# Optimization experiments

Measured on AMD Instinct MI355X. Metric: run time of the kernel, lower is better.

Reference implementation:

```python
import jax, jax.numpy as jnp
import numpy as np

N, H, G, D, FF, R = 16384, 32, 8, 128, 2, 4
GROUPS = H // G            # n_head = heads per kv group
NBAND = D // (2 * FF)      # 32


def _fold_k(t):
    # t: [N, G, D] -> (real, imag) each [N, NBAND, G*FF]; mirrors torch transpose/reshape order
    Df = D // 2
    t = jnp.swapaxes(t, -1, -2)  # [N, D, G]
    def fold(x):  # x: [N, Df, G]
        x = x.reshape(-1, NBAND, FF, G)
        x = jnp.swapaxes(x, 1, 2)          # [N, FF, NBAND, G]
        return x.reshape(-1, NBAND, G * FF)
    return fold(t[:, :Df, :]), fold(t[:, Df:, :])


def _fold_q(t):
    # t: [N, H, D] -> (real, imag) each [N, GROUPS, NBAND, G*FF]
    Df = D // 2
    t = t.reshape(-1, G, GROUPS, D).transpose(0, 2, 1, 3)  # [N, GROUPS, G, D]
    t = jnp.swapaxes(t, -1, -2)                            # [N, GROUPS, D, G]
    def fold(x):  # x: [N, GROUPS, Df, G]
        x = x.reshape(-1, GROUPS, NBAND, FF, G)
        x = jnp.swapaxes(x, 2, 3)                          # [N, GROUPS, FF, NBAND, G]
        return x.reshape(-1, GROUPS, NBAND, G * FF)
    return fold(t[:, :, :Df, :]), fold(t[:, :, Df:, :])


def setup_inputs() -> dict:
    key = jax.random.key(0)
    ks = jax.random.split(key, 5)
    return {
        "q": jax.random.normal(ks[0], (N, H, D), jnp.float32),
        "k": jax.random.normal(ks[1], (N, G, D), jnp.float32),
        "v": jax.random.normal(ks[2], (N, G, D), jnp.float32),
        "qk_index_proj": 0.02 * jax.random.normal(ks[3], (NBAND, G * FF, FF), jnp.float32),
        "v_transform": 0.02 * jax.random.normal(ks[4], (H, D, R), jnp.float32),
    }


def reference(q, k, v, qk_index_proj, v_transform):
    # index_k: fold K, project per-band, concat real/imag -> [N, D]
    kr_re, kr_im = _fold_k(k)
    kr_re_p = jnp.einsum('bnf,nfr->bnr', kr_re, qk_index_proj)
    kr_im_p = jnp.einsum('bnf,nfr->bnr', kr_im, qk_index_proj)
    index_k = jnp.concatenate(
        [kr_re_p.reshape(-1, NBAND * FF), kr_im_p.reshape(-1, NBAND * FF)], axis=-1)

    # index_q: fold Q, project per-band, concat real/imag -> [N, GROUPS, D]
    qr_re, qr_im = _fold_q(q)
    qr_re_p = jnp.einsum('tgnf,nfr->tgnr', qr_re, qk_index_proj)
    qr_im_p = jnp.einsum('tgnf,nfr->tgnr', qr_im, qk_index_proj)
    index_q = jnp.concatenate(
        [qr_re_p.reshape(-1, GROUPS, NBAND * FF), qr_im_p.reshape(-1, GROUPS, NBAND * FF)], axis=-1)

    # weights: low-rank V transform + L2 norm -> [N, GROUPS]
    v_h = jnp.repeat(v, GROUPS, axis=1)                     # [N, H, D]
    w = jnp.einsum('nhd,hdr->nhr', v_h, v_transform)        # [N, H, R]
    w = w.reshape(-1, G, GROUPS, R).transpose(0, 2, 1, 3).reshape(-1, GROUPS, G * R)
    weights = jnp.linalg.norm(w.astype(jnp.float32), axis=-1)
    return index_q, index_k, weights
```

## Files before the change

kernel.cpp:

```cpp
#include <hip/hip_runtime.h>

#define NN 16384
#define HH 32
#define GG 8
#define DD 128
#define RR 4
#define NGROUPS 4
#define NBAND 32


__global__ __launch_bounds__(256) void idxer_kernel(
    const float* __restrict__ q, const float* __restrict__ k,
    const float* __restrict__ v, const float* __restrict__ proj,
    const float* __restrict__ vt, float* __restrict__ out)
{
    const int b = blockIdx.x;
    const int tid = threadIdx.x;

    __shared__ float sq[HH * DD];
    __shared__ float sk[GG * DD];
    __shared__ float sv[GG * DD];
    __shared__ float sproj[NBAND * 33];
    __shared__ float sw[HH];

    {
        const float4* q4 = (const float4*)(q + (size_t)b * (HH * DD));
        float4* s4 = (float4*)sq;
        #pragma unroll
        for (int i = 0; i < 4; ++i) s4[tid + 256 * i] = q4[tid + 256 * i];
        const float4* k4 = (const float4*)(k + (size_t)b * (GG * DD));
        ((float4*)sk)[tid] = k4[tid];
        const float4* v4 = (const float4*)(v + (size_t)b * (GG * DD));
        ((float4*)sv)[tid] = v4[tid];
        #pragma unroll
        for (int i = 0; i < 4; ++i) {
            int p = tid + 256 * i;
            sproj[(p >> 5) * 33 + (p & 31)] = proj[p];
        }
    }
    __syncthreads();

    {
        const int group = tid >> 6;
        const int im = (tid >> 5) & 1;
        const int n = tid & 31;
        const int dbase = (n & 15) * 4 + (n >> 4) + im * 64;
        float acc0 = 0.f, acc1 = 0.f;
        #pragma unroll
        for (int j = 0; j < 16; ++j) {
            const int d = dbase + (j >> 3) * 2;
            const int head = (j & 7) * 4 + group;
            const float qv = sq[head * DD + d];
            acc0 += qv * sproj[n * 33 + j * 2];
            acc1 += qv * sproj[n * 33 + j * 2 + 1];
        }
        float2* o2 = (float2*)out;
        o2[(size_t)b * 256 + group * 64 + im * 32 + n] = make_float2(acc0, acc1);
    }

    if (tid < 64) {
        const int im = tid >> 5;
        const int n = tid & 31;
        const int dbase = (n & 15) * 4 + (n >> 4) + im * 64;
        float acc0 = 0.f, acc1 = 0.f;
        #pragma unroll
        for (int j = 0; j < 16; ++j) {
            const int d = dbase + (j >> 3) * 2;
            const int g = j & 7;
            const float kv = sk[g * DD + d];
            acc0 += kv * sproj[n * 33 + j * 2];
            acc1 += kv * sproj[n * 33 + j * 2 + 1];
        }
        float2* o2 = (float2*)(out + (size_t)NN * 512);
        o2[(size_t)b * 64 + im * 32 + n] = make_float2(acc0, acc1);
    }

    {
        const int h = tid >> 3;
        const int s = tid & 7;
        const int g = h >> 2;
        const float4* vt4 = (const float4*)vt;
        float a0 = 0.f, a1 = 0.f, a2 = 0.f, a3 = 0.f;
        #pragma unroll
        for (int i = 0; i < 16; ++i) {
            const int d = i * 8 + s;
            const float4 w4 = vt4[h * DD + d];
            const float vv = sv[g * DD + d];
            a0 += vv * w4.x; a1 += vv * w4.y; a2 += vv * w4.z; a3 += vv * w4.w;
        }
        #pragma unroll
        for (int off = 4; off >= 1; off >>= 1) {
            a0 += __shfl_down(a0, off, 8);
            a1 += __shfl_down(a1, off, 8);
            a2 += __shfl_down(a2, off, 8);
            a3 += __shfl_down(a3, off, 8);
        }
        if (s == 0) sw[h] = a0 * a0 + a1 * a1 + a2 * a2 + a3 * a3;
    }
    __syncthreads();

    if (tid < NGROUPS) {
        float acc = 0.f;
        #pragma unroll
        for (int g = 0; g < 8; ++g) acc += sw[g * 4 + tid];
        out[(size_t)NN * 512 + (size_t)NN * 128 + (size_t)b * 4 + tid] = sqrtf(acc);
    }
}

extern "C" void kernel_launch(void* const* d_in, const int* in_sizes, int n_in,
                              void* d_out, int out_size, void* d_ws, size_t ws_size,
                              hipStream_t stream) {
    const float* q    = (const float*)d_in[0];
    const float* k    = (const float*)d_in[1];
    const float* v    = (const float*)d_in[2];
    const float* proj = (const float*)d_in[3];
    const float* vt   = (const float*)d_in[4];
    float* out = (float*)d_out;
    idxer_kernel<<<NN, 256, 0, stream>>>(q, k, v, proj, vt, out);
}
```

Before: 447.1 us.

## Process eight tokens per block, stream q/k from global, reuse proj and v_transform

Each block now handles eight tokens instead of one. The per-token setup cost (loading the proj table and the v_transform slice held in registers) is paid once per block rather than once per token. Q and K are read directly from global memory as float4 into registers instead of being staged through shared memory, and only V is staged. The final cross-head reduction for the weights uses wave shuffles instead of a second barrier and shared-memory pass. In exchange, each thread does more serial work, the grid has fewer blocks, and register pressure rises from holding 16 float4 values.

```diff
diff --git a/kernel.cpp b/kernel.cpp
--- a/kernel.cpp
+++ b/kernel.cpp
@@ -1,12 +1,8 @@
 #include <hip/hip_runtime.h>
 
 #define NN 16384
-#define HH 32
-#define GG 8
-#define DD 128
-#define RR 4
-#define NGROUPS 4
-#define NBAND 32
+#define TT 8
+#define NBLK (NN / TT)
 
 
 __global__ __launch_bounds__(256) void idxer_kernel(
@@ -14,96 +10,118 @@
     const float* __restrict__ v, const float* __restrict__ proj,
     const float* __restrict__ vt, float* __restrict__ out)
 {
-    const int b = blockIdx.x;
     const int tid = threadIdx.x;
+    const int t0 = blockIdx.x * TT;
 
-    __shared__ float sq[HH * DD];
-    __shared__ float sk[GG * DD];
-    __shared__ float sv[GG * DD];
-    __shared__ float sproj[NBAND * 33];
-    __shared__ float sw[HH];
+    __shared__ __align__(16) float sproj[32 * 34];
+    __shared__ __align__(16) float sv[TT][8 * 132];
 
     {
-        const float4* q4 = (const float4*)(q + (size_t)b * (HH * DD));
-        float4* s4 = (float4*)sq;
+        const float4* pv4 = (const float4*)v;
+        float4 vbuf[TT];
         #pragma unroll
-        for (int i = 0; i < 4; ++i) s4[tid + 256 * i] = q4[tid + 256 * i];
-        const float4* k4 = (const float4*)(k + (size_t)b * (GG * DD));
-        ((float4*)sk)[tid] = k4[tid];
-        const float4* v4 = (const float4*)(v + (size_t)b * (GG * DD));
-        ((float4*)sv)[tid] = v4[tid];
+        for (int t = 0; t < TT; ++t)
+            vbuf[t] = pv4[(size_t)(t0 + t) * 256 + tid];
+        float pbuf[4];
+        #pragma unroll
+        for (int i = 0; i < 4; ++i) pbuf[i] = proj[tid + 256 * i];
         #pragma unroll
         for (int i = 0; i < 4; ++i) {
-            int p = tid + 256 * i;
-            sproj[(p >> 5) * 33 + (p & 31)] = proj[p];
+            const int p = tid + 256 * i;
+            sproj[(p >> 5) * 34 + (p & 31)] = pbuf[i];
         }
+        const int g = tid >> 5;
+        const int rem = (tid & 31) * 4;
+        #pragma unroll
+        for (int t = 0; t < TT; ++t)
+            *(float4*)&sv[t][g * 132 + rem] = vbuf[t];
     }
     __syncthreads();
 
     {
-        const int group = tid >> 6;
-        const int im = (tid >> 5) & 1;
-        const int n = tid & 31;
-        const int dbase = (n & 15) * 4 + (n >> 4) + im * 64;
-        float acc0 = 0.f, acc1 = 0.f;
-        #pragma unroll
-        for (int j = 0; j < 16; ++j) {
-            const int d = dbase + (j >> 3) * 2;
-            const int head = (j & 7) * 4 + group;
-            const float qv = sq[head * DD + d];
-            acc0 += qv * sproj[n * 33 + j * 2];
-            acc1 += qv * sproj[n * 33 + j * 2 + 1];
+        const int half = tid >> 7;
+        const int lt = tid & 127;
+        const int group = lt >> 5;
+        const int im = (lt >> 4) & 1;
+        const int a = lt & 15;
+        float2* o2 = (float2*)out;
+        #pragma unroll 2
+        for (int tq = 0; tq < TT / 2; ++tq) {
+            const int b = t0 + tq * 2 + half;
+            const float4* q4 = (const float4*)(q + (size_t)b * 4096);
+            float a0 = 0.f, a1 = 0.f, c0 = 0.f, c1 = 0.f;
+            #pragma unroll
+            for (int g8 = 0; g8 < 8; ++g8) {
+                const float4 qv = q4[(g8 * 4 + group) * 32 + im * 16 + a];
+                const float2 pa  = *(const float2*)&sproj[a * 34 + g8 * 2];
+                const float2 pa2 = *(const float2*)&sproj[a * 34 + 16 + g8 * 2];
+                const float2 pb  = *(const float2*)&sproj[(a + 16) * 34 + g8 * 2];
+                const float2 pb2 = *(const float2*)&sproj[(a + 16) * 34 + 16 + g8 * 2];
+                a0 += qv.x * pa.x + qv.z * pa2.x;
+                a1 += qv.x * pa.y + qv.z * pa2.y;
+                c0 += qv.y * pb.x + qv.w * pb2.x;
+                c1 += qv.y * pb.y + qv.w * pb2.y;
+            }
+            o2[(size_t)b * 256 + group * 64 + im * 32 + a]      = make_float2(a0, a1);
+            o2[(size_t)b * 256 + group * 64 + im * 32 + a + 16] = make_float2(c0, c1);
         }
-        float2* o2 = (float2*)out;
-        o2[(size_t)b * 256 + group * 64 + im * 32 + n] = make_float2(acc0, acc1);
-    }
-
-    if (tid < 64) {
-        const int im = tid >> 5;
-        const int n = tid & 31;
-        const int dbase = (n & 15) * 4 + (n >> 4) + im * 64;
-        float acc0 = 0.f, acc1 = 0.f;
-        #pragma unroll
-        for (int j = 0; j < 16; ++j) {
-            const int d = dbase + (j >> 3) * 2;
-            const int g = j & 7;
-            const float kv = sk[g * DD + d];
-            acc0 += kv * sproj[n * 33 + j * 2];
-            acc1 += kv * sproj[n * 33 + j * 2 + 1];
-        }
-        float2* o2 = (float2*)(out + (size_t)NN * 512);
-        o2[(size_t)b * 64 + im * 32 + n] = make_float2(acc0, acc1);
     }
 
     {
-        const int h = tid >> 3;
+        const int tsub = tid >> 5;
+        const int im = (tid >> 4) & 1;
+        const int a = tid & 15;
+        const int b = t0 + tsub;
+        const float4* k4 = (const float4*)(k + (size_t)b * 1024);
+        float a0 = 0.f, a1 = 0.f, c0 = 0.f, c1 = 0.f;
+        #pragma unroll
+        for (int g = 0; g < 8; ++g) {
+            const float4 kv = k4[g * 32 + im * 16 + a];
+            const float2 pa  = *(const float2*)&sproj[a * 34 + g * 2];
+            const float2 pa2 = *(const float2*)&sproj[a * 34 + 16 + g * 2];
+            const float2 pb  = *(const float2*)&sproj[(a + 16) * 34 + g * 2];
+            const float2 pb2 = *(const float2*)&sproj[(a + 16) * 34 + 16 + g * 2];
+            a0 += kv.x * pa.x + kv.z * pa2.x;
+            a1 += kv.x * pa.y + kv.z * pa2.y;
+            c0 += kv.y * pb.x + kv.w * pb2.x;
+            c1 += kv.y * pb.y + kv.w * pb2.y;
+        }
+        float2* o2 = (float2*)(out + (size_t)NN * 512);
+        o2[(size_t)b * 64 + im * 32 + a]      = make_float2(a0, a1);
+        o2[(size_t)b * 64 + im * 32 + a + 16] = make_float2(c0, c1);
+    }
+
+    {
+        const int group = tid >> 6;
+        const int g = (tid >> 3) & 7;
         const int s = tid & 7;
-        const int g = h >> 2;
+        const int h = g * 4 + group;
         const float4* vt4 = (const float4*)vt;
-        float a0 = 0.f, a1 = 0.f, a2 = 0.f, a3 = 0.f;
+        float4 vtr[16];
         #pragma unroll
-        for (int i = 0; i < 16; ++i) {
-            const int d = i * 8 + s;
-            const float4 w4 = vt4[h * DD + d];
-            const float vv = sv[g * DD + d];
-            a0 += vv * w4.x; a1 += vv * w4.y; a2 += vv * w4.z; a3 += vv * w4.w;
+        for (int i = 0; i < 16; ++i) vtr[i] = vt4[h * 128 + i * 8 + s];
+        float* ow = out + (size_t)NN * 512 + (size_t)NN * 128;
+        #pragma unroll 2
+        for (int t = 0; t < TT; ++t) {
+            float a0 = 0.f, a1 = 0.f, a2 = 0.f, a3 = 0.f;
+            #pragma unroll
+            for (int i = 0; i < 16; ++i) {
+                const float vv = sv[t][g * 132 + i * 8 + s];
+                a0 += vv * vtr[i].x; a1 += vv * vtr[i].y;
+                a2 += vv * vtr[i].z; a3 += vv * vtr[i].w;
+            }
+            #pragma unroll
+            for (int m = 1; m <= 4; m <<= 1) {
+                a0 += __shfl_xor(a0, m);
+                a1 += __shfl_xor(a1, m);
+                a2 += __shfl_xor(a2, m);
+                a3 += __shfl_xor(a3, m);
+            }
+            float ssq = a0 * a0 + a1 * a1 + a2 * a2 + a3 * a3;
+            #pragma unroll
+            for (int m = 8; m <= 32; m <<= 1) ssq += __shfl_xor(ssq, m);
+            if ((tid & 63) == 0) ow[(size_t)(t0 + t) * 4 + group] = sqrtf(ssq);
         }
-        #pragma unroll
-        for (int off = 4; off >= 1; off >>= 1) {
-            a0 += __shfl_down(a0, off, 8);
-            a1 += __shfl_down(a1, off, 8);
-            a2 += __shfl_down(a2, off, 8);
-            a3 += __shfl_down(a3, off, 8);
-        }
-        if (s == 0) sw[h] = a0 * a0 + a1 * a1 + a2 * a2 + a3 * a3;
-    }
-    __syncthreads();
-
-    if (tid < NGROUPS) {
-        float acc = 0.f;
-        #pragma unroll
-        for (int g = 0; g < 8; ++g) acc += sw[g * 4 + tid];
-        out[(size_t)NN * 512 + (size_t)NN * 128 + (size_t)b * 4 + tid] = sqrtf(acc);
     }
 }
 
@@ -116,5 +134,5 @@
     const float* proj = (const float*)d_in[3];
     const float* vt   = (const float*)d_in[4];
     float* out = (float*)d_out;
-    idxer_kernel<<<NN, 256, 0, stream>>>(q, k, v, proj, vt, out);
+    idxer_kernel<<<NBLK, 256, 0, stream>>>(q, k, v, proj, vt, out);
 }
```

New measurement: 452.6 us. No clear change (+1.2%).
